# Performance work log

Hardware: AMD Instinct MI355X
Metric: run time of the kernel (lower is better)

Reference implementation:

```python
import jax, jax.numpy as jnp
import numpy as np

TEMPERATURE = 0.07


def setup_inputs() -> dict:
    key = jax.random.key(0)
    embeddings = jax.random.normal(key, (16384, 256), dtype=jnp.float32)
    return {"embeddings": embeddings}


def reference(embeddings) -> jnp.ndarray:
    # L2 normalize rows (torch F.normalize uses eps clamp 1e-12)
    norm = jnp.maximum(jnp.linalg.norm(embeddings, axis=1, keepdims=True), 1e-12)
    emb = embeddings / norm
    # [N, N] similarity, temperature-scaled logits
    logits = jnp.matmul(emb, emb.T) / TEMPERATURE
    # cross entropy against diagonal labels (labels[i] = i)
    logp = jax.nn.log_softmax(logits, axis=1)
    loss = -jnp.mean(jnp.diagonal(logp))
    return loss
```

## Files before the change

### kernel.cpp

```cpp
#include <hip/hip_runtime.h>
#include <hip/hip_bf16.h>

typedef __bf16 bf16;
typedef __attribute__((ext_vector_type(8))) __bf16 bf16x8;
typedef __attribute__((ext_vector_type(4))) __bf16 bf16x4;
typedef __attribute__((ext_vector_type(16))) float f32x16;

#define N_ROWS 16384
#define DIM 256
#define NT 128
#define NJC 256
#define LSTRIP 8
#define NSTRIPS 2112
#define SQK1 4.53981608f
#define LN2F 0.69314718056f

#define WS_T_OFF (N_ROWS * DIM * 2)
#define WS_D_OFF (WS_T_OFF + N_ROWS * 4)

#define GLOAD_LDS(g, l)                                        \
    __builtin_amdgcn_global_load_lds(                          \
        (const __attribute__((address_space(1))) void*)(g),    \
        (__attribute__((address_space(3))) void*)(l), 16, 0, 0)

__global__ void __launch_bounds__(256) normalize_kernel(const float* __restrict__ in,
                                                        bf16* __restrict__ out,
                                                        float* __restrict__ Tg,
                                                        float* __restrict__ Dg,
                                                        float* __restrict__ loss_out) {
    if (blockIdx.x == 0 && threadIdx.x == 0) loss_out[0] = 0.0f;
    if (blockIdx.x < 64) Tg[blockIdx.x * 256 + threadIdx.x] = 0.0f;

    const int row  = blockIdx.x * 4 + (threadIdx.x >> 6);
    const int lane = threadIdx.x & 63;
    const float4* rp = (const float4*)(in + (size_t)row * DIM);
    float4 v = rp[lane];
    float ss = v.x * v.x + v.y * v.y + v.z * v.z + v.w * v.w;
#pragma unroll
    for (int m = 1; m < 64; m <<= 1) ss += __shfl_xor(ss, m, 64);
    float inv = SQK1 / fmaxf(sqrtf(ss), 1e-12f);
    bf16x4 o;
    o[0] = (bf16)(v.x * inv);
    o[1] = (bf16)(v.y * inv);
    o[2] = (bf16)(v.z * inv);
    o[3] = (bf16)(v.w * inv);
    *(bf16x4*)(out + (size_t)row * DIM + lane * 4) = o;

    float f0 = (float)o[0], f1 = (float)o[1], f2 = (float)o[2], f3 = (float)o[3];
    float s2 = f0 * f0 + f1 * f1 + f2 * f2 + f3 * f3;
#pragma unroll
    for (int m = 1; m < 64; m <<= 1) s2 += __shfl_xor(s2, m, 64);
    if (lane == 0) Dg[row] = s2;
}

#define TREE16(R, out)                                                     \
    do {                                                                   \
        float w8[8], w4[4], w2[2], w1, g_;                                 \
        _Pragma("unroll") for (int i_ = 0; i_ < 8; ++i_) {                 \
            g_ = (lo & 16) ? R[i_] : R[i_ + 8];                            \
            w8[i_] = ((lo & 16) ? R[i_ + 8] : R[i_]) + __shfl_xor(g_, 16); \
        }                                                                  \
        _Pragma("unroll") for (int i_ = 0; i_ < 4; ++i_) {                 \
            g_ = (lo & 8) ? w8[i_] : w8[i_ + 4];                           \
            w4[i_] = ((lo & 8) ? w8[i_ + 4] : w8[i_]) + __shfl_xor(g_, 8); \
        }                                                                  \
        _Pragma("unroll") for (int i_ = 0; i_ < 2; ++i_) {                 \
            g_ = (lo & 4) ? w4[i_] : w4[i_ + 2];                           \
            w2[i_] = ((lo & 4) ? w4[i_ + 2] : w4[i_]) + __shfl_xor(g_, 4); \
        }                                                                  \
        g_ = (lo & 2) ? w2[0] : w2[1];                                     \
        w1 = ((lo & 2) ? w2[1] : w2[0]) + __shfl_xor(g_, 2);               \
        out = w1 + __shfl_xor(w1, 1);                                      \
    } while (0)

__global__ void __launch_bounds__(512, 4)
loss_kernel(const bf16* __restrict__ A, float* __restrict__ Tg) {
    __shared__ bf16 Bs0[64 * DIM];
    __shared__ bf16 Bs1[64 * DIM];
    __shared__ float CsAcc[4][LSTRIP][64];

    const int tid = threadIdx.x;
    const int w  = tid >> 6;
    const int l  = tid & 63;
    const int lo = l & 31, hi = l >> 5;
    const int rg = w >> 1;
    const int cg = w & 1;

    int it = 0, rem = blockIdx.x;
    for (;;) {
        int nch = (NJC - 2 * it + LSTRIP - 1) >> 3;
        if (rem < nch) break;
        rem -= nch;
        ++it;
    }
    const int jc0 = 2 * it + rem * LSTRIP;
    const int jc1 = (jc0 + LSTRIP < NJC) ? (jc0 + LSTRIP) : NJC;

    bf16x8 af[16];
    {
        const bf16* ap = A + (size_t)(it * 128 + rg * 32 + lo) * DIM + hi * 8;
#pragma unroll
        for (int k = 0; k < 16; ++k)
            af[k] = *(const volatile bf16x8*)(ap + k * 16);
    }

    float s0[16];
#pragma unroll
    for (int r = 0; r < 16; ++r) s0[r] = 0.f;

    const int s_dma = l & 31;
    const int rl    = l >> 5;
    int vo[4];
#pragma unroll
    for (int q = 0; q < 4; ++q) {
        const int c = (s_dma & 24) | ((s_dma & 7) ^ ((q * 2 + rl) & 7));
        vo[q] = rl * DIM + c * 8;
    }

    const int rbase = (cg * 32 + lo) * DIM;
    const int mx7 = lo & 7;

#define ISSUE(jcn, BUF)                                                      \
    do {                                                                     \
        const bf16* tb_ = A + (size_t)((jcn) * 64 + w * 8) * DIM;            \
        bf16* lb_ = &BUF[(w * 8) * DIM];                                     \
        _Pragma("unroll") for (int q_ = 0; q_ < 4; ++q_) {                   \
            GLOAD_LDS(tb_ + (q_ * 2) * DIM + vo[q_],                         \
                      lb_ + (q_ * 2) * DIM);                                 \
        }                                                                    \
    } while (0)

#define TILE_BODY(BR, BW, jc, t)                                             \
    do {                                                                     \
        asm volatile("s_barrier" ::: "memory");                              \
        if ((jc) + 1 < jc1) {                                                \
            ISSUE((jc) + 1, BW);                                             \
            asm volatile("s_waitcnt vmcnt(4)" ::: "memory");                 \
        } else {                                                             \
            asm volatile("s_waitcnt vmcnt(0)" ::: "memory");                 \
        }                                                                    \
        asm volatile("s_barrier" ::: "memory");                              \
        f32x16 c0;                                                           \
        _Pragma("unroll") for (int r_ = 0; r_ < 16; ++r_) c0[r_] = 0.f;      \
        _Pragma("unroll") for (int k_ = 0; k_ < 16; ++k_) {                  \
            const int cc_ = k_ * 2 + hi;                                     \
            const int slot_ = (cc_ & 24) | ((cc_ & 7) ^ mx7);                \
            bf16x8 b_ = *(const bf16x8*)&BR[rbase + slot_ * 8];              \
            c0 = __builtin_amdgcn_mfma_f32_32x32x16_bf16(af[k_], b_, c0, 0, 0, 0); \
        }                                                                    \
        float cs_ = 0.f;                                                     \
        _Pragma("unroll") for (int r_ = 0; r_ < 16; ++r_) {                  \
            float e_ = __builtin_amdgcn_exp2f(c0[r_]);                       \
            s0[r_] += e_;                                                    \
            cs_ += e_;                                                       \
        }                                                                    \
        cs_ += __shfl_xor(cs_, 32);                                          \
        if (hi == 0) CsAcc[rg][t][cg * 32 + lo] = cs_;                       \
    } while (0)

    ISSUE(jc0, Bs0);
    int jc = jc0;
    while (jc < jc1) {
        TILE_BODY(Bs0, Bs1, jc, jc - jc0);
        ++jc;
        if (jc >= jc1) break;
        TILE_BODY(Bs1, Bs0, jc, jc - jc0);
        ++jc;
    }

    float t0;
    TREE16(s0, t0);
    const int r = (lo >> 1) & 15;
    const int rowoff = (r & 3) + 8 * (r >> 2) + 4 * hi;
    if ((l & 1) == 0)
        atomicAdd(&Tg[it * 128 + rg * 32 + rowoff], t0);

    __syncthreads();
    const int nt_strip = jc1 - jc0;
    for (int i = tid; i < nt_strip * 64; i += 512) {
        const int t = i >> 6, col = i & 63;
        if (((jc0 + t) >> 1) != it) {
            atomicAdd(&Tg[(jc0 + t) * 64 + col],
                      CsAcc[0][t][col] + CsAcc[1][t][col] +
                      CsAcc[2][t][col] + CsAcc[3][t][col]);
        }
    }
#undef ISSUE
#undef TILE_BODY
}

__global__ void __launch_bounds__(256) final_kernel(const float* __restrict__ Tg,
                                                    const float* __restrict__ Dg,
                                                    float* __restrict__ out) {
    __shared__ float red[4];
    const int i = blockIdx.x * 256 + threadIdx.x;
    float c = LN2F * (__log2f(Tg[i]) - Dg[i]) * (1.0f / (float)N_ROWS);
#pragma unroll
    for (int m = 1; m < 64; m <<= 1) c += __shfl_xor(c, m, 64);
    if ((threadIdx.x & 63) == 0) red[threadIdx.x >> 6] = c;
    __syncthreads();
    if (threadIdx.x == 0)
        atomicAdd(out, red[0] + red[1] + red[2] + red[3]);
}

extern "C" void kernel_launch(void* const* d_in, const int* in_sizes, int n_in,
                              void* d_out, int out_size, void* d_ws, size_t ws_size,
                              hipStream_t stream) {
    const float* emb = (const float*)d_in[0];
    float* out = (float*)d_out;
    bf16* Abf = (bf16*)d_ws;
    float* Tg = (float*)((char*)d_ws + WS_T_OFF);
    float* Dg = (float*)((char*)d_ws + WS_D_OFF);

    hipLaunchKernelGGL(normalize_kernel, dim3(N_ROWS / 4), dim3(256), 0, stream,
                       emb, Abf, Tg, Dg, out);
    hipLaunchKernelGGL(loss_kernel, dim3(NSTRIPS), dim3(512), 0, stream,
                       Abf, Tg);
    hipLaunchKernelGGL(final_kernel, dim3(N_ROWS / 256), dim3(256), 0, stream,
                       Tg, Dg, out);
}
```

Baseline: 169.3 us.

## Shrink loss-kernel tiles to 32-column B blocks with 256-thread blocks and direct column atomics

The loss kernel changes from 512-thread blocks with 64-column B tiles to 256-thread blocks with 32-column B tiles. Each of the four waves now owns 32 rows, and strips lengthen to 16 tiles, with the strip schedule recomputed so the same 2112 blocks still cover the upper triangle. The shared-memory CsAcc staging and the end-of-block column reduction are removed. Each wave instead atomically adds its per-tile column sums straight to global memory, and s_setprio is raised around the MFMA loop. This halves LDS use per block, which may allow more blocks per CU, and drops a barrier phase, at the cost of four times more global atomics for column sums.

```diff
diff --git a/kernel.cpp b/kernel.cpp
--- a/kernel.cpp
+++ b/kernel.cpp
@@ -8,9 +8,8 @@
 
 #define N_ROWS 16384
 #define DIM 256
-#define NT 128
-#define NJC 256
-#define LSTRIP 8
+#define NJC 512
+#define LSTRIP 16
 #define NSTRIPS 2112
 #define SQK1 4.53981608f
 #define LN2F 0.69314718056f
@@ -73,32 +72,29 @@
         out = w1 + __shfl_xor(w1, 1);                                      \
     } while (0)
 
-__global__ void __launch_bounds__(512, 4)
+__global__ void __launch_bounds__(256, 4)
 loss_kernel(const bf16* __restrict__ A, float* __restrict__ Tg) {
-    __shared__ bf16 Bs0[64 * DIM];
-    __shared__ bf16 Bs1[64 * DIM];
-    __shared__ float CsAcc[4][LSTRIP][64];
+    __shared__ bf16 Bs0[32 * DIM];
+    __shared__ bf16 Bs1[32 * DIM];
 
     const int tid = threadIdx.x;
     const int w  = tid >> 6;
     const int l  = tid & 63;
     const int lo = l & 31, hi = l >> 5;
-    const int rg = w >> 1;
-    const int cg = w & 1;
 
     int it = 0, rem = blockIdx.x;
     for (;;) {
-        int nch = (NJC - 2 * it + LSTRIP - 1) >> 3;
+        const int nch = 32 - (it >> 2);
         if (rem < nch) break;
         rem -= nch;
         ++it;
     }
-    const int jc0 = 2 * it + rem * LSTRIP;
+    const int jc0 = 4 * it + rem * LSTRIP;
     const int jc1 = (jc0 + LSTRIP < NJC) ? (jc0 + LSTRIP) : NJC;
 
     bf16x8 af[16];
     {
-        const bf16* ap = A + (size_t)(it * 128 + rg * 32 + lo) * DIM + hi * 8;
+        const bf16* ap = A + (size_t)(it * 128 + w * 32 + lo) * DIM + hi * 8;
 #pragma unroll
         for (int k = 0; k < 16; ++k)
             af[k] = *(const volatile bf16x8*)(ap + k * 16);
@@ -117,12 +113,12 @@
         vo[q] = rl * DIM + c * 8;
     }
 
-    const int rbase = (cg * 32 + lo) * DIM;
+    const int rbase = lo * DIM;
     const int mx7 = lo & 7;
 
 #define ISSUE(jcn, BUF)                                                      \
     do {                                                                     \
-        const bf16* tb_ = A + (size_t)((jcn) * 64 + w * 8) * DIM;            \
+        const bf16* tb_ = A + (size_t)((jcn) * 32 + w * 8) * DIM;            \
         bf16* lb_ = &BUF[(w * 8) * DIM];                                     \
         _Pragma("unroll") for (int q_ = 0; q_ < 4; ++q_) {                   \
             GLOAD_LDS(tb_ + (q_ * 2) * DIM + vo[q_],                         \
@@ -130,7 +126,7 @@
         }                                                                    \
     } while (0)
 
-#define TILE_BODY(BR, BW, jc, t)                                             \
+#define TILE_BODY(BR, BW, jc)                                                \
     do {                                                                     \
         asm volatile("s_barrier" ::: "memory");                              \
         if ((jc) + 1 < jc1) {                                                \
@@ -142,12 +138,14 @@
         asm volatile("s_barrier" ::: "memory");                              \
         f32x16 c0;                                                           \
         _Pragma("unroll") for (int r_ = 0; r_ < 16; ++r_) c0[r_] = 0.f;      \
+        __builtin_amdgcn_s_setprio(1);                                       \
         _Pragma("unroll") for (int k_ = 0; k_ < 16; ++k_) {                  \
             const int cc_ = k_ * 2 + hi;                                     \
             const int slot_ = (cc_ & 24) | ((cc_ & 7) ^ mx7);                \
             bf16x8 b_ = *(const bf16x8*)&BR[rbase + slot_ * 8];              \
             c0 = __builtin_amdgcn_mfma_f32_32x32x16_bf16(af[k_], b_, c0, 0, 0, 0); \
         }                                                                    \
+        __builtin_amdgcn_s_setprio(0);                                       \
         float cs_ = 0.f;                                                     \
         _Pragma("unroll") for (int r_ = 0; r_ < 16; ++r_) {                  \
             float e_ = __builtin_amdgcn_exp2f(c0[r_]);                       \
@@ -155,16 +153,18 @@
             cs_ += e_;                                                       \
         }                                                                    \
         cs_ += __shfl_xor(cs_, 32);                                          \
-        if (hi == 0) CsAcc[rg][t][cg * 32 + lo] = cs_;                       \
+                             \
+        if (((jc) >> 2) != it && hi == 0)                                    \
+            atomicAdd(&Tg[(jc) * 32 + lo], cs_);                             \
     } while (0)
 
     ISSUE(jc0, Bs0);
     int jc = jc0;
     while (jc < jc1) {
-        TILE_BODY(Bs0, Bs1, jc, jc - jc0);
+        TILE_BODY(Bs0, Bs1, jc);
         ++jc;
         if (jc >= jc1) break;
-        TILE_BODY(Bs1, Bs0, jc, jc - jc0);
+        TILE_BODY(Bs1, Bs0, jc);
         ++jc;
     }
 
@@ -173,18 +173,7 @@
     const int r = (lo >> 1) & 15;
     const int rowoff = (r & 3) + 8 * (r >> 2) + 4 * hi;
     if ((l & 1) == 0)
-        atomicAdd(&Tg[it * 128 + rg * 32 + rowoff], t0);
-
-    __syncthreads();
-    const int nt_strip = jc1 - jc0;
-    for (int i = tid; i < nt_strip * 64; i += 512) {
-        const int t = i >> 6, col = i & 63;
-        if (((jc0 + t) >> 1) != it) {
-            atomicAdd(&Tg[(jc0 + t) * 64 + col],
-                      CsAcc[0][t][col] + CsAcc[1][t][col] +
-                      CsAcc[2][t][col] + CsAcc[3][t][col]);
-        }
-    }
+        atomicAdd(&Tg[it * 128 + w * 32 + rowoff], t0);
 #undef ISSUE
 #undef TILE_BODY
 }
@@ -214,7 +203,7 @@
 
     hipLaunchKernelGGL(normalize_kernel, dim3(N_ROWS / 4), dim3(256), 0, stream,
                        emb, Abf, Tg, Dg, out);
-    hipLaunchKernelGGL(loss_kernel, dim3(NSTRIPS), dim3(512), 0, stream,
+    hipLaunchKernelGGL(loss_kernel, dim3(NSTRIPS), dim3(256), 0, stream,
                        Abf, Tg);
     hipLaunchKernelGGL(final_kernel, dim3(N_ROWS / 256), dim3(256), 0, stream,
                        Tg, Dg, out);
```

After: 161.6 us. 4.6% less time.
